# Performance work log

Hardware: AMD Instinct MI355X
Metric: run time of the kernel (lower is better)

Reference implementation:

```python
import jax, jax.numpy as jnp
import numpy as np

N = 10000      # nodes
E = 100000     # edges
H = 256        # hidden_dim
HEADS = 4
HD = H // HEADS
G = 8          # graphs in batch
SPG = N // G   # nodes per graph (equal-size graphs -> to_dense_batch is a reshape)
IN = 16        # in_dim
PE = 5         # pe_dims
ED = 8         # edge_dim
OUT = 4        # out_dim
L = 5          # num_layers


def setup_inputs() -> dict:
    key = jax.random.key(0)
    ks = iter(jax.random.split(key, 64))
    rn = lambda shape, s=0.05: jax.random.normal(next(ks), shape, jnp.float32) * s
    inp = {}
    inp['x'] = jax.random.normal(next(ks), (N, IN), jnp.float32)
    inp['pe'] = jax.random.normal(next(ks), (N, PE), jnp.float32)
    inp['edge_attr'] = jax.random.normal(next(ks), (E, ED), jnp.float32)
    inp['edge_index'] = jax.random.randint(next(ks), (2, E), 0, N, jnp.int32)
    inp['batch'] = (jnp.arange(N) // SPG).astype(jnp.int32)
    # node encoders (3 node types), stacked
    inp['enc_w1'] = rn((3, IN + PE, H)); inp['enc_b1'] = rn((3, H))
    inp['enc_w2'] = rn((3, H, H));       inp['enc_b2'] = rn((3, H))
    # edge encoder
    inp['ee_w1'] = rn((ED, H)); inp['ee_b1'] = rn((H,))
    inp['ee_w2'] = rn((H, H));  inp['ee_b2'] = rn((H,))
    # per-layer edge / node update MLPs, stacked over layers
    inp['eu_w1'] = rn((L, 3 * H, H)); inp['eu_b1'] = rn((L, H))
    inp['eu_w2'] = rn((L, H, H));     inp['eu_b2'] = rn((L, H))
    inp['nu_w1'] = rn((L, 2 * H, H)); inp['nu_b1'] = rn((L, H))
    inp['nu_w2'] = rn((L, H, H));     inp['nu_b2'] = rn((L, H))
    # MultiheadAttention (combined in-proj + out-proj)
    inp['qkv_w'] = rn((H, 3 * H)); inp['qkv_b'] = rn((3 * H,))
    inp['out_w'] = rn((H, H));     inp['out_b'] = rn((H,))
    # fusion MLP
    inp['fu_w1'] = rn((H, H)); inp['fu_b1'] = rn((H,))
    inp['fu_w2'] = rn((H, H)); inp['fu_b2'] = rn((H,))
    # decoders (3 node types)
    inp['dec_w1'] = rn((3, H, H));   inp['dec_b1'] = rn((3, H))
    inp['dec_w2'] = rn((3, H, OUT)); inp['dec_b2'] = rn((3, OUT))
    return inp


def _mlp(z, w1, b1, w2, b2):
    return jnp.maximum(z @ w1 + b1, 0.0) @ w2 + b2


def reference(x, pe, edge_attr, edge_index, batch,
              enc_w1, enc_b1, enc_w2, enc_b2,
              ee_w1, ee_b1, ee_w2, ee_b2,
              eu_w1, eu_b1, eu_w2, eu_b2,
              nu_w1, nu_b1, nu_w2, nu_b2,
              qkv_w, qkv_b, out_w, out_b,
              fu_w1, fu_b1, fu_w2, fu_b2,
              dec_w1, dec_b1, dec_w2, dec_b2):
    n = x.shape[0]
    node_types = (jnp.clip(jnp.round(x[:, 2] * 3.0), 1.0, 3.0).astype(jnp.int32) - 1)
    rng_n = jnp.arange(n)

    # node encoding: run all 3 type-MLPs, select per node (masked dispatch in torch)
    inp = jnp.concatenate([x, pe], axis=-1)                       # [N, IN+PE]
    hid = jnp.maximum(jnp.einsum('ni,tih->tnh', inp, enc_w1) + enc_b1[:, None, :], 0.0)
    h_all = jnp.einsum('tnh,tho->tno', hid, enc_w2) + enc_b2[:, None, :]  # [3,N,H]
    h_nodes = h_all[node_types, rng_n]                            # [N, H]

    h_edges = _mlp(edge_attr, ee_w1, ee_b1, ee_w2, ee_b2)         # [E, H]

    src, dst = edge_index[0], edge_index[1]
    for l in range(L):
        e_in = jnp.concatenate([h_nodes[src], h_nodes[dst], h_edges], axis=-1)  # [E,3H]
        h_edges = h_edges + _mlp(e_in, eu_w1[l], eu_b1[l], eu_w2[l], eu_b2[l])
        m_node = jax.ops.segment_sum(h_edges, dst, num_segments=n)              # index_add_
        n_in = jnp.concatenate([h_nodes, m_node], axis=-1)                      # [N,2H]
        h_nodes = h_nodes + _mlp(n_in, nu_w1[l], nu_b1[l], nu_w2[l], nu_b2[l])

    # global attention: equal-size graphs -> to_dense_batch is a reshape, mask all-true
    xp = h_nodes.reshape(G, SPG, H)
    qkv = xp @ qkv_w + qkv_b                                      # [G,S,3H]
    q, k, v = jnp.split(qkv, 3, axis=-1)
    split_heads = lambda t: t.reshape(G, SPG, HEADS, HD).transpose(0, 2, 1, 3)
    q, k, v = split_heads(q), split_heads(k), split_heads(v)
    scale = 1.0 / np.sqrt(HD).astype(np.float32)
    att = jax.nn.softmax(jnp.einsum('ghsd,ghtd->ghst', q, k) * scale, axis=-1)
    o = jnp.einsum('ghst,ghtd->ghsd', att, v).transpose(0, 2, 1, 3).reshape(G, SPG, H)
    glob = (xp + (o @ out_w + out_b)).reshape(n, H)

    h = _mlp(h_nodes + glob, fu_w1, fu_b1, fu_w2, fu_b2)

    dhid = jnp.maximum(jnp.einsum('nh,tho->tno', h, dec_w1) + dec_b1[:, None, :], 0.0)
    out_all = jnp.einsum('tno,tok->tnk', dhid, dec_w2) + dec_b2[:, None, :]     # [3,N,OUT]
    return out_all[node_types, rng_n]
```

## Files before the change

kernel.cpp:

```cpp
#include <hip/hip_runtime.h>
#include <hip/hip_bf16.h>
#include <math.h>

#define NN 10000
#define NE 100000
#define SPGc 1250
#define NG 8
#define NL 5
#define ECHK 50000

__device__ __forceinline__ int imin(int a, int b) { return a < b ? a : b; }

__global__ __launch_bounds__(256) void k_types(const float* __restrict__ x, int* __restrict__ types) {
    int i = blockIdx.x * 256 + threadIdx.x;
    if (i < NN) {
        float v = rintf(x[(size_t)i * 16 + 2] * 3.0f);
        v = fminf(fmaxf(v, 1.0f), 3.0f);
        types[i] = (int)v - 1;
    }
}

__global__ __launch_bounds__(256) void k_hist(const int* __restrict__ dst, int* __restrict__ deg) {
    int e = blockIdx.x * 256 + threadIdx.x;
    if (e < NE) atomicAdd(&deg[dst[e]], 1);
}

__global__ __launch_bounds__(256) void k_scan(const int* __restrict__ deg, int* __restrict__ row_ptr,
                                              int* __restrict__ cursor) {
    __shared__ int buf[256];
    int tid = threadIdx.x;
    int base = 0;
    for (int c = 0; c < NN; c += 256) {
        int i = c + tid;
        int v = (i < NN) ? deg[i] : 0;
        buf[tid] = v;
        __syncthreads();
        for (int off = 1; off < 256; off <<= 1) {
            int t = (tid >= off) ? buf[tid - off] : 0;
            __syncthreads();
            buf[tid] += t;
            __syncthreads();
        }
        if (i < NN) {
            row_ptr[i + 1] = base + buf[tid];
            cursor[i] = base + buf[tid] - v;
        }
        __syncthreads();
        base += buf[255];
        __syncthreads();
    }
    if (tid == 0) row_ptr[0] = 0;
}

__global__ __launch_bounds__(256) void k_scatter(const int* __restrict__ dst, int* __restrict__ cursor,
                                                 int* __restrict__ csr) {
    int e = blockIdx.x * 256 + threadIdx.x;
    if (e < NE) {
        int p = atomicAdd(&cursor[dst[e]], 1);
        csr[p] = e;
    }
}

__global__ __launch_bounds__(256) void k_enc(const float* __restrict__ x, const float* __restrict__ pe,
        const int* __restrict__ types,
        const float* __restrict__ w1, const float* __restrict__ b1,
        const float* __restrict__ w2, const float* __restrict__ b2,
        float* __restrict__ h_nodes) {
    int n = blockIdx.x;
    int j = threadIdx.x;
    __shared__ float inp[21];
    __shared__ float hid[256];
    if (j < 16) inp[j] = x[(size_t)n * 16 + j];
    else if (j < 21) inp[j] = pe[(size_t)n * 5 + (j - 16)];
    __syncthreads();
    int t = types[n];
    const float* W1 = w1 + (size_t)t * 21 * 256;
    float a = b1[t * 256 + j];
    #pragma unroll
    for (int i = 0; i < 21; ++i) a = fmaf(inp[i], W1[i * 256 + j], a);
    hid[j] = fmaxf(a, 0.f);
    __syncthreads();
    const float* W2 = w2 + (size_t)t * 256 * 256;
    float o = b2[t * 256 + j];
    #pragma unroll 8
    for (int k = 0; k < 256; ++k) o = fmaf(hid[k], W2[k * 256 + j], o);
    h_nodes[(size_t)n * 256 + j] = o;
}

__global__ __launch_bounds__(256) void gemm64(int Mrows, int K, int Nout,
        const float* __restrict__ A0, int lda,
        const float* __restrict__ W, const float* __restrict__ bias,
        float* __restrict__ C) {
    __shared__ __align__(16) float As[16][68];
    __shared__ __align__(16) float Ws[16][64];
    int tid = threadIdx.x;
    int tx = tid & 15, ty = tid >> 4;
    int blockRow = blockIdx.x * 64;
    int ncol0 = blockIdx.y * 64;
    float acc[4][4];
    #pragma unroll
    for (int i = 0; i < 4; ++i)
        #pragma unroll
        for (int j = 0; j < 4; ++j) acc[i][j] = 0.f;

    for (int k0 = 0; k0 < K; k0 += 16) {
        #pragma unroll
        for (int i = 0; i < 4; ++i) {
            int id = tid + 256 * i;
            int kk = id & 15, r = id >> 4;
            int grow = blockRow + r;
            int k = k0 + kk;
            float v = 0.f;
            if (grow < Mrows && k < K) v = A0[(size_t)grow * lda + k];
            As[kk][r] = v;
        }
        #pragma unroll
        for (int i = 0; i < 4; ++i) {
            int id = tid + 256 * i;
            int c = id & 63, kk = id >> 6;
            int k = k0 + kk;
            Ws[kk][c] = (k < K) ? W[(size_t)k * Nout + ncol0 + c] : 0.f;
        }
        __syncthreads();
        #pragma unroll
        for (int kk = 0; kk < 16; ++kk) {
            const float4 a4 = *(const float4*)&As[kk][ty << 2];
            const float4 w4 = *(const float4*)&Ws[kk][tx << 2];
            float av[4] = {a4.x, a4.y, a4.z, a4.w};
            float wv[4] = {w4.x, w4.y, w4.z, w4.w};
            #pragma unroll
            for (int i = 0; i < 4; ++i)
                #pragma unroll
                for (int j = 0; j < 4; ++j)
                    acc[i][j] = fmaf(av[i], wv[j], acc[i][j]);
        }
        __syncthreads();
    }
    #pragma unroll
    for (int i = 0; i < 4; ++i) {
        int grow = blockRow + (ty << 2) + i;
        if (grow >= Mrows) continue;
        size_t base = (size_t)grow * Nout + ncol0 + (tx << 2);
        #pragma unroll
        for (int j = 0; j < 4; ++j)
            C[base + j] = fmaxf(acc[i][j] + bias[ncol0 + (tx << 2) + j], 0.f);
    }
}

template<bool GATHER, bool RELU, bool RES>
__global__ __launch_bounds__(256) void gemm_big(int Mrows,
        const float* __restrict__ A,
        const float* __restrict__ W, const float* __restrict__ bias,
        const int* __restrict__ gs, const int* __restrict__ gd, int gOfs,
        const float* __restrict__ Pa, const float* __restrict__ Pb,
        const float* __restrict__ Res, float* __restrict__ C) {
    __shared__ __align__(16) float As[16][132];
    __shared__ __align__(16) float Ws[16][16][20];
    int tid = threadIdx.x;
    int blockRow = blockIdx.x * 128;
    int rg = tid >> 4, cg = tid & 15;
    int srow = tid >> 1, skh = (tid & 1) * 8;
    int swk = tid >> 4, scg = tid & 15;
    float acc[8][16];
    #pragma unroll
    for (int i = 0; i < 8; ++i)
        #pragma unroll
        for (int n = 0; n < 16; ++n) acc[i][n] = 0.f;

    for (int k0 = 0; k0 < 256; k0 += 16) {
        {
            int arow = imin(blockRow + srow, Mrows - 1);
            const float* ap = A + (size_t)arow * 256 + k0 + skh;
            float4 a0 = *(const float4*)ap;
            float4 a1 = *(const float4*)(ap + 4);
            As[skh + 0][srow] = a0.x; As[skh + 1][srow] = a0.y;
            As[skh + 2][srow] = a0.z; As[skh + 3][srow] = a0.w;
            As[skh + 4][srow] = a1.x; As[skh + 5][srow] = a1.y;
            As[skh + 6][srow] = a1.z; As[skh + 7][srow] = a1.w;
        }
        {
            const float* wp = W + (size_t)(k0 + swk) * 256 + scg * 16;
            *(float4*)&Ws[swk][scg][0]  = *(const float4*)(wp + 0);
            *(float4*)&Ws[swk][scg][4]  = *(const float4*)(wp + 4);
            *(float4*)&Ws[swk][scg][8]  = *(const float4*)(wp + 8);
            *(float4*)&Ws[swk][scg][12] = *(const float4*)(wp + 12);
        }
        __syncthreads();
        #pragma unroll
        for (int kk = 0; kk < 16; ++kk) {
            const float4 a0 = *(const float4*)&As[kk][rg << 3];
            const float4 a1 = *(const float4*)&As[kk][(rg << 3) + 4];
            float av[8] = {a0.x, a0.y, a0.z, a0.w, a1.x, a1.y, a1.z, a1.w};
            const float4 w0 = *(const float4*)&Ws[kk][cg][0];
            const float4 w1 = *(const float4*)&Ws[kk][cg][4];
            const float4 w2 = *(const float4*)&Ws[kk][cg][8];
            const float4 w3 = *(const float4*)&Ws[kk][cg][12];
            float wv[16] = {w0.x, w0.y, w0.z, w0.w, w1.x, w1.y, w1.z, w1.w,
                            w2.x, w2.y, w2.z, w2.w, w3.x, w3.y, w3.z, w3.w};
            #pragma unroll
            for (int i = 0; i < 8; ++i)
                #pragma unroll
                for (int j = 0; j < 16; ++j)
                    acc[i][j] = fmaf(av[i], wv[j], acc[i][j]);
        }
        __syncthreads();
    }
    int colb = cg << 4;
    #pragma unroll
    for (int i = 0; i < 8; ++i) {
        int row = blockRow + (rg << 3) + i;
        if (row >= Mrows) continue;
        size_t base = (size_t)row * 256 + colb;
        const float* par = nullptr;
        const float* pbr = nullptr;
        if (GATHER) {
            par = Pa + (size_t)gs[gOfs + row] * 256 + colb;
            pbr = Pb + (size_t)gd[gOfs + row] * 256 + colb;
        }
        #pragma unroll
        for (int q = 0; q < 4; ++q) {
            const float4 b4 = *(const float4*)(bias + colb + q * 4);
            float v[4] = {acc[i][q * 4 + 0] + b4.x, acc[i][q * 4 + 1] + b4.y,
                          acc[i][q * 4 + 2] + b4.z, acc[i][q * 4 + 3] + b4.w};
            if (GATHER) {
                const float4 pa4 = *(const float4*)(par + q * 4);
                const float4 pb4 = *(const float4*)(pbr + q * 4);
                v[0] += pa4.x + pb4.x; v[1] += pa4.y + pb4.y;
                v[2] += pa4.z + pb4.z; v[3] += pa4.w + pb4.w;
            }
            if (RELU) {
                v[0] = fmaxf(v[0], 0.f); v[1] = fmaxf(v[1], 0.f);
                v[2] = fmaxf(v[2], 0.f); v[3] = fmaxf(v[3], 0.f);
            }
            if (RES) {
                const float4 rv = *(const float4*)(Res + base + q * 4);
                v[0] += rv.x; v[1] += rv.y; v[2] += rv.z; v[3] += rv.w;
            }
            float4 o; o.x = v[0]; o.y = v[1]; o.z = v[2]; o.w = v[3];
            *(float4*)(C + base + q * 4) = o;
        }
    }
}

template<int AMODE, bool RELU, bool HASRES, bool HASBIAS>
__global__ __launch_bounds__(256) void gemm_f32(int Mrows, int K, int Nout,
        const float* __restrict__ A0, const float* __restrict__ A1, int lda,
        const float* __restrict__ W, const float* __restrict__ bias,
        const float* __restrict__ ResF, float resScale,
        float* __restrict__ C, int zW, int zC) {
    __shared__ __align__(16) float As[16][68];
    __shared__ __align__(16) float Ws[16][16][10];
    int tid = threadIdx.x;
    int blockRow = blockIdx.x * 64;
    int ncol0 = blockIdx.y * 128;
    W += (size_t)blockIdx.z * zW;
    C += (size_t)blockIdx.z * zC;
    int rg = tid >> 4, cg = tid & 15;
    int sar = tid >> 2, sak = (tid & 3) * 4;
    int swk = tid >> 4, scg = tid & 15;
    float acc[4][8];
    #pragma unroll
    for (int i = 0; i < 4; ++i)
        #pragma unroll
        for (int n = 0; n < 8; ++n) acc[i][n] = 0.f;

    for (int k0 = 0; k0 < K; k0 += 16) {
        {
            int arow = imin(blockRow + sar, Mrows - 1);
            float4 av;
            if (AMODE == 0) {
                av = *(const float4*)(A0 + (size_t)arow * lda + k0 + sak);
            } else {
                int k = k0 + sak;
                av = (k < 256) ? *(const float4*)(A0 + (size_t)arow * 256 + k)
                               : *(const float4*)(A1 + (size_t)arow * 256 + (k - 256));
            }
            As[sak + 0][sar] = av.x;
            As[sak + 1][sar] = av.y;
            As[sak + 2][sar] = av.z;
            As[sak + 3][sar] = av.w;
        }
        {
            const float* wp = W + (size_t)(k0 + swk) * Nout + ncol0 + scg * 8;
            *(float4*)&Ws[swk][scg][0] = *(const float4*)(wp + 0);
            *(float4*)&Ws[swk][scg][4] = *(const float4*)(wp + 4);
        }
        __syncthreads();
        #pragma unroll
        for (int kk = 0; kk < 16; ++kk) {
            const float4 a4 = *(const float4*)&As[kk][rg << 2];
            float av[4] = {a4.x, a4.y, a4.z, a4.w};
            const float4 w0 = *(const float4*)&Ws[kk][cg][0];
            const float4 w1 = *(const float4*)&Ws[kk][cg][4];
            float wv[8] = {w0.x, w0.y, w0.z, w0.w, w1.x, w1.y, w1.z, w1.w};
            #pragma unroll
            for (int i = 0; i < 4; ++i)
                #pragma unroll
                for (int j = 0; j < 8; ++j)
                    acc[i][j] = fmaf(av[i], wv[j], acc[i][j]);
        }
        __syncthreads();
    }
    #pragma unroll
    for (int i = 0; i < 4; ++i) {
        int grow = blockRow + (rg << 2) + i;
        if (grow >= Mrows) continue;
        size_t crow = (size_t)grow;
        int colb = ncol0 + (cg << 3);
        #pragma unroll
        for (int q = 0; q < 2; ++q) {
            float v[4];
            #pragma unroll
            for (int j = 0; j < 4; ++j) v[j] = acc[i][q * 4 + j];
            if (HASBIAS) {
                const float4 b4 = *(const float4*)(bias + colb + q * 4);
                v[0] += b4.x; v[1] += b4.y; v[2] += b4.z; v[3] += b4.w;
            }
            if (RELU) {
                v[0] = fmaxf(v[0], 0.f); v[1] = fmaxf(v[1], 0.f);
                v[2] = fmaxf(v[2], 0.f); v[3] = fmaxf(v[3], 0.f);
            }
            if (HASRES) {
                const float4 rv = *(const float4*)(ResF + crow * Nout + colb + q * 4);
                v[0] += resScale * rv.x; v[1] += resScale * rv.y;
                v[2] += resScale * rv.z; v[3] += resScale * rv.w;
            }
            float4 o; o.x = v[0]; o.y = v[1]; o.z = v[2]; o.w = v[3];
            *(float4*)(C + crow * Nout + colb + q * 4) = o;
        }
    }
}

__global__ __launch_bounds__(256) void k_mnode(const float* __restrict__ h_edges,
        const int* __restrict__ row_ptr, const int* __restrict__ csr, float* __restrict__ m_node) {
    int n = blockIdx.x * 4 + (threadIdx.x >> 6);
    int lane = threadIdx.x & 63;
    if (n >= NN) return;
    float a0 = 0.f, a1 = 0.f, a2 = 0.f, a3 = 0.f;
    int s = row_ptr[n], e = row_ptr[n + 1];
    for (int i = s; i < e; ++i) {
        int ed = csr[i];
        const float4 v = *(const float4*)(h_edges + (size_t)ed * 256 + (lane << 2));
        a0 += v.x; a1 += v.y; a2 += v.z; a3 += v.w;
    }
    float4 r; r.x = a0; r.y = a1; r.z = a2; r.w = a3;
    *(float4*)(m_node + (size_t)n * 256 + (lane << 2)) = r;
}

__global__ __launch_bounds__(256) void k_attn(const float* __restrict__ qkv, float* __restrict__ obuf) {
    int gh = blockIdx.y;
    int g = gh >> 2, h = gh & 3;
    int q0 = blockIdx.x * 64;
    int tid = threadIdx.x;
    int r = tid >> 2, q4 = tid & 3;
    int d0 = q4 * 16;
    __shared__ __align__(16) float Ks[32][68];
    __shared__ __align__(16) float Vs[32][68];
    const float* base = qkv + (size_t)g * SPGc * 768;
    int my_s = q0 + r;
    bool rowok = my_s < SPGc;
    float qreg[16];
    #pragma unroll
    for (int dd = 0; dd < 16; ++dd) qreg[dd] = 0.f;
    if (rowok) {
        const float* qp = base + (size_t)my_s * 768 + h * 64 + d0;
        #pragma unroll
        for (int dd = 0; dd < 16; ++dd) qreg[dd] = qp[dd];
    }
    float m = -1e30f, l = 0.f;
    float oacc[16];
    #pragma unroll
    for (int dd = 0; dd < 16; ++dd) oacc[dd] = 0.f;

    int srow = tid >> 3, sc8 = (tid & 7) * 8;
    for (int t0 = 0; t0 < SPGc; t0 += 32) {
        {
            int s = t0 + srow;
            float4 k0v = {0,0,0,0}, k1v = {0,0,0,0}, v0v = {0,0,0,0}, v1v = {0,0,0,0};
            if (s < SPGc) {
                const float* kp = base + (size_t)s * 768 + h * 64 + sc8;
                k0v = *(const float4*)(kp + 256);
                k1v = *(const float4*)(kp + 260);
                v0v = *(const float4*)(kp + 512);
                v1v = *(const float4*)(kp + 516);
            }
            *(float4*)&Ks[srow][sc8]     = k0v;
            *(float4*)&Ks[srow][sc8 + 4] = k1v;
            *(float4*)&Vs[srow][sc8]     = v0v;
            *(float4*)&Vs[srow][sc8 + 4] = v1v;
        }
        __syncthreads();
        float sc[32];
        #pragma unroll
        for (int j = 0; j < 32; ++j) {
            float p = 0.f;
            #pragma unroll
            for (int dd = 0; dd < 16; dd += 4) {
                const float4 k4 = *(const float4*)&Ks[j][d0 + dd];
                p = fmaf(qreg[dd], k4.x, p);
                p = fmaf(qreg[dd + 1], k4.y, p);
                p = fmaf(qreg[dd + 2], k4.z, p);
                p = fmaf(qreg[dd + 3], k4.w, p);
            }
            sc[j] = p;
        }
        #pragma unroll
        for (int j = 0; j < 32; ++j) {
            float p = sc[j];
            p += __shfl_xor(p, 1);
            p += __shfl_xor(p, 2);
            sc[j] = (t0 + j < SPGc) ? p * 0.125f : -1e30f;
        }
        float mt = sc[0];
        #pragma unroll
        for (int j = 1; j < 32; ++j) mt = fmaxf(mt, sc[j]);
        float mnew = fmaxf(m, mt);
        float f = __expf(m - mnew);
        l *= f;
        #pragma unroll
        for (int dd = 0; dd < 16; ++dd) oacc[dd] *= f;
        #pragma unroll
        for (int j = 0; j < 32; ++j) {
            float p = __expf(sc[j] - mnew);
            l += p;
            #pragma unroll
            for (int dd = 0; dd < 16; dd += 4) {
                const float4 v4 = *(const float4*)&Vs[j][d0 + dd];
                oacc[dd]     = fmaf(p, v4.x, oacc[dd]);
                oacc[dd + 1] = fmaf(p, v4.y, oacc[dd + 1]);
                oacc[dd + 2] = fmaf(p, v4.z, oacc[dd + 2]);
                oacc[dd + 3] = fmaf(p, v4.w, oacc[dd + 3]);
            }
        }
        m = mnew;
        __syncthreads();
    }
    if (rowok) {
        float rinv = 1.0f / l;
        float* op = obuf + (size_t)(g * SPGc + my_s) * 256 + h * 64 + d0;
        #pragma unroll
        for (int dd = 0; dd < 16; ++dd) op[dd] = oacc[dd] * rinv;
    }
}

__global__ __launch_bounds__(256) void k_dec(const float* __restrict__ h, const int* __restrict__ types,
        const float* __restrict__ w1, const float* __restrict__ b1,
        const float* __restrict__ w2, const float* __restrict__ b2,
        float* __restrict__ out) {
    int n = blockIdx.x;
    int j = threadIdx.x;
    __shared__ float hrow[256];
    __shared__ float dhid[256];
    hrow[j] = h[(size_t)n * 256 + j];
    __syncthreads();
    int t = types[n];
    const float* W1 = w1 + (size_t)t * 256 * 256;
    float a = b1[t * 256 + j];
    #pragma unroll 8
    for (int k = 0; k < 256; ++k) a = fmaf(hrow[k], W1[k * 256 + j], a);
    dhid[j] = fmaxf(a, 0.f);
    __syncthreads();
    int lane = j & 63, w = j >> 6;
    const float* W2 = w2 + (size_t)t * 256 * 4;
    float p = 0.f;
    #pragma unroll
    for (int q = 0; q < 4; ++q) {
        int kk = lane + 64 * q;
        p = fmaf(dhid[kk], W2[kk * 4 + w], p);
    }
    #pragma unroll
    for (int o2 = 32; o2 > 0; o2 >>= 1) p += __shfl_down(p, o2);
    if (lane == 0) out[(size_t)n * 4 + w] = p + b2[t * 4 + w];
}

extern "C" void kernel_launch(void* const* d_in, const int* in_sizes, int n_in,
                              void* d_out, int out_size, void* d_ws, size_t ws_size,
                              hipStream_t stream) {
    const float* x         = (const float*)d_in[0];
    const float* pe        = (const float*)d_in[1];
    const float* edge_attr = (const float*)d_in[2];
    const int*   eidx      = (const int*)d_in[3];
    const float* enc_w1 = (const float*)d_in[5];
    const float* enc_b1 = (const float*)d_in[6];
    const float* enc_w2 = (const float*)d_in[7];
    const float* enc_b2 = (const float*)d_in[8];
    const float* ee_w1  = (const float*)d_in[9];
    const float* ee_b1  = (const float*)d_in[10];
    const float* ee_w2  = (const float*)d_in[11];
    const float* ee_b2  = (const float*)d_in[12];
    const float* eu_w1  = (const float*)d_in[13];
    const float* eu_b1  = (const float*)d_in[14];
    const float* eu_w2  = (const float*)d_in[15];
    const float* eu_b2  = (const float*)d_in[16];
    const float* nu_w1  = (const float*)d_in[17];
    const float* nu_b1  = (const float*)d_in[18];
    const float* nu_w2  = (const float*)d_in[19];
    const float* nu_b2  = (const float*)d_in[20];
    const float* qkv_w  = (const float*)d_in[21];
    const float* qkv_b  = (const float*)d_in[22];
    const float* out_w  = (const float*)d_in[23];
    const float* out_b  = (const float*)d_in[24];
    const float* fu_w1  = (const float*)d_in[25];
    const float* fu_b1  = (const float*)d_in[26];
    const float* fu_w2  = (const float*)d_in[27];
    const float* fu_b2  = (const float*)d_in[28];
    const float* dec_w1 = (const float*)d_in[29];
    const float* dec_b1 = (const float*)d_in[30];
    const float* dec_w2 = (const float*)d_in[31];
    const float* dec_b2 = (const float*)d_in[32];

    const int* src  = eidx;
    const int* dstp = eidx + NE;

    float* ws = (float*)d_ws;
    float* h_edges = ws;
    float* region  = ws + 25600000;
    float* h_nodes = ws + 38400000;
    float* mn_ob   = ws + 40960000;
    float* nhid    = ws + 43520000;
    int* ibase   = (int*)(ws + 46080000);
    int* types   = ibase;
    int* deg     = ibase + NN;
    int* row_ptr = deg + NN;
    int* cursor  = row_ptr + NN + 1;
    int* csr     = cursor + NN;

    float* ehid = region;
    float* Pa   = mn_ob;
    float* Pb   = nhid;
    float* qkvf = region;
    float* fin  = region + 7680000;

    hipMemsetAsync(deg, 0, NN * sizeof(int), stream);
    k_types<<<(NN + 255) / 256, 256, 0, stream>>>(x, types);
    k_hist<<<(NE + 255) / 256, 256, 0, stream>>>(dstp, deg);
    k_scan<<<1, 256, 0, stream>>>(deg, row_ptr, cursor);
    k_scatter<<<(NE + 255) / 256, 256, 0, stream>>>(dstp, cursor, csr);

    k_enc<<<NN, 256, 0, stream>>>(x, pe, types, enc_w1, enc_b1, enc_w2, enc_b2, h_nodes);

    int gBig = (ECHK + 127) / 128;
    dim3 gN((NN + 63) / 64, 2);

    for (int c0 = 0; c0 < NE; c0 += ECHK) {
        gemm64<<<dim3((ECHK + 63) / 64, 4), 256, 0, stream>>>(ECHK, 8, 256,
            edge_attr + (size_t)c0 * 8, 8, ee_w1, ee_b1, ehid);
        gemm_big<false, false, false><<<gBig, 256, 0, stream>>>(ECHK,
            ehid, ee_w2, ee_b2, nullptr, nullptr, 0, nullptr, nullptr,
            nullptr, h_edges + (size_t)c0 * 256);
    }

    for (int l = 0; l < NL; ++l) {
        const float* W1 = eu_w1 + (size_t)l * 768 * 256;
        gemm_f32<0, false, false, false><<<dim3((NN + 63) / 64, 2, 2), 256, 0, stream>>>(NN, 256, 256,
            h_nodes, nullptr, 256, W1, nullptr, nullptr, 0.f, Pa, 65536, 2560000);
        for (int c0 = 0; c0 < NE; c0 += ECHK) {
            gemm_big<true, true, false><<<gBig, 256, 0, stream>>>(ECHK,
                h_edges + (size_t)c0 * 256, W1 + 131072, eu_b1 + l * 256,
                src, dstp, c0, Pa, Pb, nullptr, ehid);
            gemm_big<false, false, true><<<gBig, 256, 0, stream>>>(ECHK,
                ehid, eu_w2 + (size_t)l * 65536, eu_b2 + l * 256,
                nullptr, nullptr, 0, nullptr, nullptr,
                h_edges + (size_t)c0 * 256, h_edges + (size_t)c0 * 256);
        }
        k_mnode<<<(NN + 3) / 4, 256, 0, stream>>>(h_edges, row_ptr, csr, mn_ob);
        gemm_f32<2, true, false, true><<<gN, 256, 0, stream>>>(NN, 512, 256,
            h_nodes, mn_ob, 256, nu_w1 + (size_t)l * 131072, nu_b1 + l * 256,
            nullptr, 0.f, nhid, 0, 0);
        gemm_f32<0, false, true, true><<<gN, 256, 0, stream>>>(NN, 256, 256,
            nhid, nullptr, 256, nu_w2 + (size_t)l * 65536, nu_b2 + l * 256,
            h_nodes, 1.f, h_nodes, 0, 0);
    }

    gemm_f32<0, false, false, true><<<dim3((NN + 63) / 64, 6), 256, 0, stream>>>(NN, 256, 768,
        h_nodes, nullptr, 256, qkv_w, qkv_b, nullptr, 0.f, qkvf, 0, 0);

    dim3 ga((SPGc + 63) / 64, NG * 4);
    k_attn<<<ga, 256, 0, stream>>>(qkvf, mn_ob);

    gemm_f32<0, false, true, true><<<gN, 256, 0, stream>>>(NN, 256, 256,
        mn_ob, nullptr, 256, out_w, out_b, h_nodes, 2.f, fin, 0, 0);
    gemm_f32<0, true, false, true><<<gN, 256, 0, stream>>>(NN, 256, 256,
        fin, nullptr, 256, fu_w1, fu_b1, nullptr, 0.f, nhid, 0, 0);
    gemm_f32<0, false, false, true><<<gN, 256, 0, stream>>>(NN, 256, 256,
        nhid, nullptr, 256, fu_w2, fu_b2, nullptr, 0.f, mn_ob, 0, 0);

    k_dec<<<NN, 256, 0, stream>>>(mn_ob, types, dec_w1, dec_b1, dec_w2, dec_b2, (float*)d_out);
}
```

Before: 4.070 ms.

## Double-buffer attention K/V tiles and process all edges in one chunk

The attention kernel now prefetches the next K/V tile into registers while the current tile is computed, using double-buffered shared memory. It also uses a tree reduction for the max and split partial sums for the softmax denominator. The host side processes all edges in a single chunk when the workspace is large enough, which halves the edge GEMM launches and enlarges their grids. The cost is more shared memory and registers in attention, plus a larger workspace requirement, with a fallback to 50000-edge chunks when the workspace is too small.

```diff
diff --git a/kernel.cpp b/kernel.cpp
--- a/kernel.cpp
+++ b/kernel.cpp
@@ -7,9 +7,9 @@
 #define SPGc 1250
 #define NG 8
 #define NL 5
-#define ECHK 50000
 
 __device__ __forceinline__ int imin(int a, int b) { return a < b ? a : b; }
+static inline int hmin(int a, int b) { return a < b ? a : b; }
 
 __global__ __launch_bounds__(256) void k_types(const float* __restrict__ x, int* __restrict__ types) {
     int i = blockIdx.x * 256 + threadIdx.x;
@@ -354,8 +354,8 @@
     int tid = threadIdx.x;
     int r = tid >> 2, q4 = tid & 3;
     int d0 = q4 * 16;
-    __shared__ __align__(16) float Ks[32][68];
-    __shared__ __align__(16) float Vs[32][68];
+    __shared__ __align__(16) float Ks[2][32][68];
+    __shared__ __align__(16) float Vs[2][32][68];
     const float* base = qkv + (size_t)g * SPGc * 768;
     int my_s = q0 + r;
     bool rowok = my_s < SPGc;
@@ -373,30 +373,47 @@
     for (int dd = 0; dd < 16; ++dd) oacc[dd] = 0.f;
 
     int srow = tid >> 3, sc8 = (tid & 7) * 8;
-    for (int t0 = 0; t0 < SPGc; t0 += 32) {
-        {
-            int s = t0 + srow;
-            float4 k0v = {0,0,0,0}, k1v = {0,0,0,0}, v0v = {0,0,0,0}, v1v = {0,0,0,0};
+    const int NIT = (SPGc + 31) / 32;
+    float4 pk0, pk1, pv0, pv1;
+
+    {
+        int s = srow;
+        pk0 = pk1 = pv0 = pv1 = (float4){0.f, 0.f, 0.f, 0.f};
+        if (s < SPGc) {
+            const float* kp = base + (size_t)s * 768 + h * 64 + sc8;
+            pk0 = *(const float4*)(kp + 256);
+            pk1 = *(const float4*)(kp + 260);
+            pv0 = *(const float4*)(kp + 512);
+            pv1 = *(const float4*)(kp + 516);
+        }
+    }
+    *(float4*)&Ks[0][srow][sc8]     = pk0;
+    *(float4*)&Ks[0][srow][sc8 + 4] = pk1;
+    *(float4*)&Vs[0][srow][sc8]     = pv0;
+    *(float4*)&Vs[0][srow][sc8 + 4] = pv1;
+    __syncthreads();
+
+    for (int it = 0; it < NIT; ++it) {
+        int t0 = it * 32;
+        int cb = it & 1;
+        if (it + 1 < NIT) {
+            int s = (it + 1) * 32 + srow;
+            pk0 = pk1 = pv0 = pv1 = (float4){0.f, 0.f, 0.f, 0.f};
             if (s < SPGc) {
                 const float* kp = base + (size_t)s * 768 + h * 64 + sc8;
-                k0v = *(const float4*)(kp + 256);
-                k1v = *(const float4*)(kp + 260);
-                v0v = *(const float4*)(kp + 512);
-                v1v = *(const float4*)(kp + 516);
-            }
-            *(float4*)&Ks[srow][sc8]     = k0v;
-            *(float4*)&Ks[srow][sc8 + 4] = k1v;
-            *(float4*)&Vs[srow][sc8]     = v0v;
-            *(float4*)&Vs[srow][sc8 + 4] = v1v;
-        }
-        __syncthreads();
+                pk0 = *(const float4*)(kp + 256);
+                pk1 = *(const float4*)(kp + 260);
+                pv0 = *(const float4*)(kp + 512);
+                pv1 = *(const float4*)(kp + 516);
+            }
+        }
         float sc[32];
         #pragma unroll
         for (int j = 0; j < 32; ++j) {
             float p = 0.f;
             #pragma unroll
             for (int dd = 0; dd < 16; dd += 4) {
-                const float4 k4 = *(const float4*)&Ks[j][d0 + dd];
+                const float4 k4 = *(const float4*)&Ks[cb][j][d0 + dd];
                 p = fmaf(qreg[dd], k4.x, p);
                 p = fmaf(qreg[dd + 1], k4.y, p);
                 p = fmaf(qreg[dd + 2], k4.z, p);
@@ -411,29 +428,45 @@
             p += __shfl_xor(p, 2);
             sc[j] = (t0 + j < SPGc) ? p * 0.125f : -1e30f;
         }
-        float mt = sc[0];
-        #pragma unroll
-        for (int j = 1; j < 32; ++j) mt = fmaxf(mt, sc[j]);
+        float t16[16];
+        #pragma unroll
+        for (int j = 0; j < 16; ++j) t16[j] = fmaxf(sc[j], sc[j + 16]);
+        float t8[8];
+        #pragma unroll
+        for (int j = 0; j < 8; ++j) t8[j] = fmaxf(t16[j], t16[j + 8]);
+        float t4[4];
+        #pragma unroll
+        for (int j = 0; j < 4; ++j) t4[j] = fmaxf(t8[j], t8[j + 4]);
+        float mt = fmaxf(fmaxf(t4[0], t4[1]), fmaxf(t4[2], t4[3]));
         float mnew = fmaxf(m, mt);
         float f = __expf(m - mnew);
-        l *= f;
         #pragma unroll
         for (int dd = 0; dd < 16; ++dd) oacc[dd] *= f;
+        float lp[4] = {0.f, 0.f, 0.f, 0.f};
         #pragma unroll
         for (int j = 0; j < 32; ++j) {
             float p = __expf(sc[j] - mnew);
-            l += p;
+            lp[j & 3] += p;
             #pragma unroll
             for (int dd = 0; dd < 16; dd += 4) {
-                const float4 v4 = *(const float4*)&Vs[j][d0 + dd];
+                const float4 v4 = *(const float4*)&Vs[cb][j][d0 + dd];
                 oacc[dd]     = fmaf(p, v4.x, oacc[dd]);
                 oacc[dd + 1] = fmaf(p, v4.y, oacc[dd + 1]);
                 oacc[dd + 2] = fmaf(p, v4.z, oacc[dd + 2]);
                 oacc[dd + 3] = fmaf(p, v4.w, oacc[dd + 3]);
             }
         }
+        l = l * f + ((lp[0] + lp[1]) + (lp[2] + lp[3]));
         m = mnew;
         __syncthreads();
+        if (it + 1 < NIT) {
+            int nb = cb ^ 1;
+            *(float4*)&Ks[nb][srow][sc8]     = pk0;
+            *(float4*)&Ks[nb][srow][sc8 + 4] = pk1;
+            *(float4*)&Vs[nb][srow][sc8]     = pv0;
+            *(float4*)&Vs[nb][srow][sc8 + 4] = pv1;
+            __syncthreads();
+        }
     }
     if (rowok) {
         float rinv = 1.0f / l;
@@ -513,23 +546,38 @@
     const int* dstp = eidx + NE;
 
     float* ws = (float*)d_ws;
+    const size_t needFull = ((size_t)58880000 + 140016) * 4 + (1u << 20);
+    bool full = (ws_size >= needFull);
+
     float* h_edges = ws;
-    float* region  = ws + 25600000;
-    float* h_nodes = ws + 38400000;
-    float* mn_ob   = ws + 40960000;
-    float* nhid    = ws + 43520000;
-    int* ibase   = (int*)(ws + 46080000);
+    float *ehid, *h_nodes, *mn_ob, *nhid;
+    int* ibase;
+    int echk;
+    if (full) {
+        ehid    = ws + 25600000;
+        h_nodes = ws + 51200000;
+        mn_ob   = ws + 53760000;
+        nhid    = ws + 56320000;
+        ibase   = (int*)(ws + 58880000);
+        echk    = NE;
+    } else {
+        ehid    = ws + 25600000;
+        h_nodes = ws + 38400000;
+        mn_ob   = ws + 40960000;
+        nhid    = ws + 43520000;
+        ibase   = (int*)(ws + 46080000);
+        echk    = 50000;
+    }
     int* types   = ibase;
     int* deg     = ibase + NN;
     int* row_ptr = deg + NN;
     int* cursor  = row_ptr + NN + 1;
     int* csr     = cursor + NN;
 
-    float* ehid = region;
     float* Pa   = mn_ob;
     float* Pb   = nhid;
-    float* qkvf = region;
-    float* fin  = region + 7680000;
+    float* qkvf = ehid;
+    float* fin  = ehid + 7680000;
 
     hipMemsetAsync(deg, 0, NN * sizeof(int), stream);
     k_types<<<(NN + 255) / 256, 256, 0, stream>>>(x, types);
@@ -539,13 +587,13 @@
 
     k_enc<<<NN, 256, 0, stream>>>(x, pe, types, enc_w1, enc_b1, enc_w2, enc_b2, h_nodes);
 
-    int gBig = (ECHK + 127) / 128;
     dim3 gN((NN + 63) / 64, 2);
 
-    for (int c0 = 0; c0 < NE; c0 += ECHK) {
-        gemm64<<<dim3((ECHK + 63) / 64, 4), 256, 0, stream>>>(ECHK, 8, 256,
+    for (int c0 = 0; c0 < NE; c0 += echk) {
+        int mrows = hmin(echk, NE - c0);
+        gemm64<<<dim3((mrows + 63) / 64, 4), 256, 0, stream>>>(mrows, 8, 256,
             edge_attr + (size_t)c0 * 8, 8, ee_w1, ee_b1, ehid);
-        gemm_big<false, false, false><<<gBig, 256, 0, stream>>>(ECHK,
+        gemm_big<false, false, false><<<(mrows + 127) / 128, 256, 0, stream>>>(mrows,
             ehid, ee_w2, ee_b2, nullptr, nullptr, 0, nullptr, nullptr,
             nullptr, h_edges + (size_t)c0 * 256);
     }
@@ -554,11 +602,12 @@
         const float* W1 = eu_w1 + (size_t)l * 768 * 256;
         gemm_f32<0, false, false, false><<<dim3((NN + 63) / 64, 2, 2), 256, 0, stream>>>(NN, 256, 256,
             h_nodes, nullptr, 256, W1, nullptr, nullptr, 0.f, Pa, 65536, 2560000);
-        for (int c0 = 0; c0 < NE; c0 += ECHK) {
-            gemm_big<true, true, false><<<gBig, 256, 0, stream>>>(ECHK,
+        for (int c0 = 0; c0 < NE; c0 += echk) {
+            int mrows = hmin(echk, NE - c0);
+            gemm_big<true, true, false><<<(mrows + 127) / 128, 256, 0, stream>>>(mrows,
                 h_edges + (size_t)c0 * 256, W1 + 131072, eu_b1 + l * 256,
                 src, dstp, c0, Pa, Pb, nullptr, ehid);
-            gemm_big<false, false, true><<<gBig, 256, 0, stream>>>(ECHK,
+            gemm_big<false, false, true><<<(mrows + 127) / 128, 256, 0, stream>>>(mrows,
                 ehid, eu_w2 + (size_t)l * 65536, eu_b2 + l * 256,
                 nullptr, nullptr, 0, nullptr, nullptr,
                 h_edges + (size_t)c0 * 256, h_edges + (size_t)c0 * 256);
```

Measured after the change: 5.524 ms. 35.7% more time.
